# Kernel tuning notes

Measured on AMD Instinct MI355X. Metric: run time of the kernel, lower is better.

## Reference

```python
import jax, jax.numpy as jnp
import numpy as np

B, S, H = 128, 1000, 256


def setup_inputs() -> dict:
    key = jax.random.key(0)
    ks = jax.random.split(key, 15)
    sc = 1.0 / np.sqrt(H)
    f = lambda k, shape: (jax.random.normal(k, shape, jnp.float32) * sc)
    return dict(
        static_hidden=jax.random.normal(ks[0], (B, S, H), jnp.float32),
        state_embedding=jax.random.normal(ks[1], (B, 1, H), jnp.float32),
        decoder_hidden=jax.random.normal(ks[2], (B, 1, H), jnp.float32),
        target_hidden=jax.random.normal(ks[3], (B, 1, H), jnp.float32),
        last_hh=jax.random.normal(ks[4], (1, B, H), jnp.float32),
        W_ih=f(ks[5], (3 * H, H)),
        W_hh=f(ks[6], (3 * H, H)),
        b_ih=f(ks[7], (3 * H,)),
        b_hh=f(ks[8], (3 * H,)),
        v_attn_enc=f(ks[9], (H,)),
        W_attn_enc=f(ks[10], (H, 2 * H)),
        v_attn_tgt=f(ks[11], (H,)),
        W_attn_tgt=f(ks[12], (H, 2 * H)),
        v_ptr=f(ks[13], (H,)),
        W_ptr=f(ks[14], (H, 3 * H)),
    )


def _attention(static, dec, v, W):
    # static: [B,S,H], dec: [B,1,H] -> softmax attention over S
    hid = jnp.concatenate([static, jnp.broadcast_to(dec, static.shape)], axis=2)  # [B,S,2H]
    t = jnp.tanh(jnp.einsum('hk,bsk->bhs', W, hid))  # [B,H,S]
    return jax.nn.softmax(jnp.einsum('h,bhs->bs', v, t), axis=1)  # [B,S]


def _gru_step(x, h, Wih, Whh, bih, bhh):
    # single-layer single-step torch GRU semantics; x,h: [B,H]
    gi = x @ Wih.T + bih
    gh = h @ Whh.T + bhh
    ir, iz, ig = jnp.split(gi, 3, axis=-1)
    hr, hz, hg = jnp.split(gh, 3, axis=-1)
    r = jax.nn.sigmoid(ir + hr)
    z = jax.nn.sigmoid(iz + hz)
    n = jnp.tanh(ig + r * hg)
    return (1.0 - z) * n + z * h


def _pointer_branch(static, state_emb, attn, v, W):
    context = jnp.einsum('bs,bsh->bh', attn, static)[:, None, :]  # [B,1,H]
    energy = jnp.concatenate(
        [static,
         jnp.broadcast_to(context, static.shape),
         jnp.broadcast_to(state_emb, static.shape)], axis=2)  # [B,S,3H]
    return jnp.einsum('h,bhs->bs', v, jnp.tanh(jnp.einsum('hk,bsk->bhs', W, energy)))


def reference(static_hidden, state_embedding, decoder_hidden, target_hidden, last_hh,
              W_ih, W_hh, b_ih, b_hh,
              v_attn_enc, W_attn_enc, v_attn_tgt, W_attn_tgt, v_ptr, W_ptr):
    # GRU step (dropout is identity in eval / p=0.0)
    h_new = _gru_step(decoder_hidden[:, 0, :], last_hh[0], W_ih, W_hh, b_ih, b_hh)
    rnn_out = h_new[:, None, :]  # [B,1,H]
    last_hh_new = h_new[None]    # [1,B,H]

    enc_attn = _attention(static_hidden, rnn_out, v_attn_enc, W_attn_enc)
    probs = _pointer_branch(static_hidden, state_embedding, enc_attn, v_ptr, W_ptr)

    tgt_attn = _attention(static_hidden, target_hidden, v_attn_tgt, W_attn_tgt)
    # NOTE: original code reuses self.v / self.W (not v_target/W_taret) for the
    # target branch energy -- replicated faithfully.
    probs_target = _pointer_branch(static_hidden, state_embedding, tgt_attn, v_ptr, W_ptr)

    return (5.0 * probs + probs_target, last_hh_new)
```

## Files before the change

kernel.cpp:

```cpp
#include <hip/hip_runtime.h>
#include <hip/hip_bf16.h>
#include <stdint.h>
#include <stddef.h>

#define Bn 128
#define Sn 1000
#define SP 1024
#define Hn 256

typedef __bf16 bf16;
typedef __bf16 bf16x8 __attribute__((ext_vector_type(8)));
typedef __bf16 bf16x4 __attribute__((ext_vector_type(4)));
typedef __bf16 bf16x2 __attribute__((ext_vector_type(2)));
typedef float  f32x4  __attribute__((ext_vector_type(4)));

typedef __attribute__((address_space(1))) const unsigned int* gas1;
typedef __attribute__((address_space(3))) unsigned int* las3;

__device__ __forceinline__ float fast_tanh(float x){
  return 1.0f - 2.0f / (__expf(2.0f * x) + 1.0f);
}
__device__ __forceinline__ float fast_sigmoid(float x){
  return 1.0f / (1.0f + __expf(-x));
}
__device__ __forceinline__ float dot4(float4 a, float4 b){
  return a.x*b.x + a.y*b.y + a.z*b.z + a.w*b.w;
}

__global__ void k0a_convert(const float* __restrict__ stat, bf16* __restrict__ Abf){
  int p = blockIdx.x * 256 + threadIdx.x;
  int row = p >> 5;
  int ch  = p & 31;
  int s = row & (SP - 1);
  int b = row >> 10;
  float4 f0 = make_float4(0.f,0.f,0.f,0.f), f1 = f0;
  if (s < Sn){
    const float4* src = (const float4*)(stat + ((size_t)(b*Sn + s))*Hn + ch*8);
    f0 = src[0]; f1 = src[1];
  }
  bf16x8 v;
  v[0]=(bf16)f0.x; v[1]=(bf16)f0.y; v[2]=(bf16)f0.z; v[3]=(bf16)f0.w;
  v[4]=(bf16)f1.x; v[5]=(bf16)f1.y; v[6]=(bf16)f1.z; v[7]=(bf16)f1.w;
  *(bf16x8*)(Abf + (size_t)row*Hn + ch*8) = v;
}

__global__ void k0b_weights(const float* __restrict__ We, const float* __restrict__ Wt,
                            const float* __restrict__ Wp, bf16* __restrict__ Wcb){
  int t = blockIdx.x * 256 + threadIdx.x;
  int r = t >> 8, c = t & 255;
  float val;
  if (r < 256)       val = We[r*512 + c];
  else if (r < 512)  val = Wt[(r-256)*512 + c];
  else               val = Wp[(r-512)*768 + c];
  Wcb[t] = (bf16)val;
}

__global__ void k1_gru(const float* __restrict__ dec, const float* __restrict__ lhh,
                       const float* __restrict__ tgt, const float* __restrict__ se,
                       const float* __restrict__ Wih, const float* __restrict__ Whh,
                       const float* __restrict__ bih, const float* __restrict__ bhh,
                       const float* __restrict__ We,  const float* __restrict__ Wt,
                       const float* __restrict__ Wp,
                       float* __restrict__ out_hh, float* __restrict__ d_enc,
                       float* __restrict__ d_tgt,  float* __restrict__ c3){
  __shared__ __align__(16) float xs[256], hs[256], hn[256], ts[256], ss[256];
  int b = blockIdx.x, t = threadIdx.x;
  xs[t] = dec[b*256 + t];
  hs[t] = lhh[b*256 + t];
  ts[t] = tgt[b*256 + t];
  ss[t] = se[b*256 + t];
  __syncthreads();

  const float4* wir = (const float4*)(Wih + (size_t)t*256);
  const float4* wiz = (const float4*)(Wih + (size_t)(256+t)*256);
  const float4* wig = (const float4*)(Wih + (size_t)(512+t)*256);
  const float4* whr = (const float4*)(Whh + (size_t)t*256);
  const float4* whz = (const float4*)(Whh + (size_t)(256+t)*256);
  const float4* whg = (const float4*)(Whh + (size_t)(512+t)*256);
  float gir=0.f, giz=0.f, gig=0.f, ghr=0.f, ghz=0.f, ghg=0.f;
  #pragma unroll 4
  for (int k=0;k<64;k++){
    float4 xv = ((const float4*)xs)[k];
    float4 hv = ((const float4*)hs)[k];
    gir += dot4(wir[k], xv);
    giz += dot4(wiz[k], xv);
    gig += dot4(wig[k], xv);
    ghr += dot4(whr[k], hv);
    ghz += dot4(whz[k], hv);
    ghg += dot4(whg[k], hv);
  }
  gir += bih[t];      ghr += bhh[t];
  giz += bih[256+t];  ghz += bhh[256+t];
  gig += bih[512+t];  ghg += bhh[512+t];
  float r = fast_sigmoid(gir + ghr);
  float z = fast_sigmoid(giz + ghz);
  float n = fast_tanh(gig + r*ghg);
  float h = (1.f - z)*n + z*hs[t];
  hn[t] = h;
  out_hh[b*256 + t] = h;
  __syncthreads();

  const float4* we2 = (const float4*)(We + (size_t)t*512 + 256);
  const float4* wt2 = (const float4*)(Wt + (size_t)t*512 + 256);
  const float4* wp3 = (const float4*)(Wp + (size_t)t*768 + 512);
  float de=0.f, dt=0.f, cv=0.f;
  #pragma unroll 4
  for (int k=0;k<64;k++){
    float4 hv = ((const float4*)hn)[k];
    float4 tv = ((const float4*)ts)[k];
    float4 sv = ((const float4*)ss)[k];
    de += dot4(we2[k], hv);
    dt += dot4(wt2[k], tv);
    cv += dot4(wp3[k], sv);
  }
  d_enc[b*256 + t] = de;
  d_tgt[b*256 + t] = dt;
  c3[b*256 + t]    = cv;
}

__global__ __launch_bounds__(256) void k2_gemm(
    const bf16* __restrict__ Abf, const bf16* __restrict__ Wcb,
    const float* __restrict__ d_enc, const float* __restrict__ d_tgt,
    const float* __restrict__ c3, const float* __restrict__ v_enc,
    const float* __restrict__ v_tgt,
    float* __restrict__ sc_e, float* __restrict__ sc_t,
    bf16* __restrict__ Aptr){
  __shared__ __align__(16) bf16 As[64*256];
  __shared__ __align__(16) bf16 Bs[128*64];
  __shared__ float scoreE[64], scoreT[64];
  int tid = threadIdx.x;
  int w = tid >> 6, l = tid & 63;
  int st = blockIdx.x, b = blockIdx.y;
  int wm = (w & 1) * 32, wn = (w >> 1) * 64;
  int lm = l & 15, q = l >> 4;

  if (tid < 64) scoreE[tid] = 0.f;
  else if (tid < 128) scoreT[tid-64] = 0.f;

  {
    const bf16* gA = Abf + ((size_t)(b*SP + st*64)) * Hn;
    int rl = w*2 + (l >> 5);
    int ch = l & 31;
    #pragma unroll
    for (int is = 0; is < 8; is++){
      int row = is*8 + rl;
      int sc_ = ch ^ (row & 7);
      __builtin_amdgcn_global_load_lds((gas1)(gA + (size_t)row*256 + sc_*8),
                                       (las3)(&As[(is*8 + w*2)*256]), 16, 0, 0);
    }
  }

  int rB8 = w*8 + (l >> 3);
  int chB = l & 7;

  for (int nc = 0; nc < 6; nc++){
    f32x4 acc[2][4];
    #pragma unroll
    for (int i=0;i<2;i++)
      #pragma unroll
      for (int j=0;j<4;j++) acc[i][j] = (f32x4){0.f,0.f,0.f,0.f};

    for (int kt = 0; kt < 4; kt++){
      __syncthreads();
      #pragma unroll
      for (int is = 0; is < 4; is++){
        int row = is*32 + rB8;
        int sc_ = chB ^ (row & 7);
        __builtin_amdgcn_global_load_lds((gas1)(Wcb + ((size_t)(nc*128 + row))*256 + kt*64 + sc_*8),
                                         (las3)(&Bs[(is*32 + w*8)*64]), 16, 0, 0);
      }
      __syncthreads();
      #pragma unroll
      for (int kk = 0; kk < 64; kk += 32){
        bf16x8 af[2], bfr[4];
        int cA = kt*8 + (kk >> 3) + q;
        int cB = (kk >> 3) + q;
        #pragma unroll
        for (int i=0;i<2;i++){
          int rA = wm + i*16 + lm;
          af[i] = *(const bf16x8*)(&As[rA*256 + ((cA ^ (rA & 7)) << 3)]);
        }
        #pragma unroll
        for (int j=0;j<4;j++){
          int rB = wn + j*16 + lm;
          bfr[j] = *(const bf16x8*)(&Bs[rB*64 + ((cB ^ (rB & 7)) << 3)]);
        }
        #pragma unroll
        for (int i=0;i<2;i++)
          #pragma unroll
          for (int j=0;j<4;j++)
            acc[i][j] = __builtin_amdgcn_mfma_f32_16x16x32_bf16(af[i], bfr[j], acc[i][j], 0, 0, 0);
      }
    }

    int hb = (nc & 1) * 128;
    if (nc < 4){
      const float* vv = (nc < 2) ? v_enc : v_tgt;
      const float* db = ((nc < 2) ? d_enc : d_tgt) + b*256;
      float* sc = (nc < 2) ? scoreE : scoreT;
      float vj[4], dj[4];
      #pragma unroll
      for (int j=0;j<4;j++){
        int hh = hb + wn + j*16 + lm;
        vj[j] = vv[hh]; dj[j] = db[hh];
      }
      #pragma unroll
      for (int i=0;i<2;i++){
        #pragma unroll
        for (int r=0;r<4;r++){
          float p = 0.f;
          #pragma unroll
          for (int j=0;j<4;j++) p += vj[j] * fast_tanh(acc[i][j][r] + dj[j]);
          p += __shfl_xor(p, 1);
          p += __shfl_xor(p, 2);
          p += __shfl_xor(p, 4);
          p += __shfl_xor(p, 8);
          if (lm == 0) atomicAdd(&sc[wm + i*16 + q*4 + r], p);
        }
      }
    } else {
      int hbp = (nc - 4) * 128;
      const float* c3b = c3 + b*256;
      float cv[4]; int hhj[4];
      #pragma unroll
      for (int j=0;j<4;j++){
        hhj[j] = hbp + wn + j*16 + lm;
        cv[j] = c3b[hhj[j]];
      }
      #pragma unroll
      for (int i=0;i<2;i++){
        #pragma unroll
        for (int r=0;r<4;r++){
          int row = wm + i*16 + q*4 + r;
          int gs = st*64 + row;
          if (gs < Sn){
            size_t rb = ((size_t)(b*Sn + gs))*256;
            #pragma unroll
            for (int j=0;j<4;j++)
              Aptr[rb + hhj[j]] = (bf16)(acc[i][j][r] + cv[j]);
          }
        }
      }
    }
  }

  __syncthreads();
  if (tid < 64)       sc_e[b*SP + st*64 + tid]      = scoreE[tid];
  else if (tid < 128) sc_t[b*SP + st*64 + tid - 64] = scoreT[tid-64];
}

__global__ __launch_bounds__(1024) void k3_ctx(
    const float* __restrict__ sc_e, const float* __restrict__ sc_t,
    const bf16* __restrict__ Abf,
    float* __restrict__ ctxPE, float* __restrict__ ctxPT){
  __shared__ float attE[1024], attT[1024];
  __shared__ float redE[16], redT[16];
  __shared__ float pe[8*256], pt[8*256];
  int b = blockIdx.x, sp = blockIdx.y, t = threadIdx.x;
  int wid = t >> 6, ln = t & 63;

  float vE = (t < Sn) ? sc_e[b*SP + t] : -1e30f;
  float vT = (t < Sn) ? sc_t[b*SP + t] : -1e30f;
  float mE = vE, mT = vT;
  #pragma unroll
  for (int o=1;o<64;o<<=1){ mE = fmaxf(mE, __shfl_xor(mE,o)); mT = fmaxf(mT, __shfl_xor(mT,o)); }
  if (ln == 0){ redE[wid] = mE; redT[wid] = mT; }
  __syncthreads();
  float ME = -1e30f, MT = -1e30f;
  #pragma unroll
  for (int i=0;i<16;i++){ ME = fmaxf(ME, redE[i]); MT = fmaxf(MT, redT[i]); }
  __syncthreads();
  float eE = (t < Sn) ? __expf(vE - ME) : 0.f;
  float eT = (t < Sn) ? __expf(vT - MT) : 0.f;
  float sE = eE, sT = eT;
  #pragma unroll
  for (int o=1;o<64;o<<=1){ sE += __shfl_xor(sE,o); sT += __shfl_xor(sT,o); }
  if (ln == 0){ redE[wid] = sE; redT[wid] = sT; }
  __syncthreads();
  float SE = 0.f, ST = 0.f;
  #pragma unroll
  for (int i=0;i<16;i++){ SE += redE[i]; ST += redT[i]; }
  attE[t] = eE / SE;
  attT[t] = eT / ST;
  __syncthreads();

  int sh = t >> 7, hp = t & 127;
  const bf16* base = Abf + ((size_t)(b*SP + sp*500))*Hn + hp*2;
  float aE0=0.f, aE1=0.f, aT0=0.f, aT1=0.f;
  #pragma unroll 4
  for (int i=0;i<63;i++){
    int sl = sh + 8*i;
    if (sl < 500){
      int s = sp*500 + sl;
      float wE = attE[s], wT = attT[s];
      bf16x2 pr = *(const bf16x2*)(base + (size_t)sl*Hn);
      float p0 = (float)pr[0], p1 = (float)pr[1];
      aE0 += wE*p0; aE1 += wE*p1;
      aT0 += wT*p0; aT1 += wT*p1;
    }
  }
  pe[sh*256 + hp*2] = aE0; pe[sh*256 + hp*2+1] = aE1;
  pt[sh*256 + hp*2] = aT0; pt[sh*256 + hp*2+1] = aT1;
  __syncthreads();
  if (t < 256){
    float s = 0.f;
    #pragma unroll
    for (int i=0;i<8;i++) s += pe[i*256 + t];
    ctxPE[((size_t)(sp*Bn + b))*256 + t] = s;
  } else if (t < 512){
    int tt = t - 256;
    float s = 0.f;
    #pragma unroll
    for (int i=0;i<8;i++) s += pt[i*256 + tt];
    ctxPT[((size_t)(sp*Bn + b))*256 + tt] = s;
  }
}

__global__ void k3c_c2(const float* __restrict__ ctxPE, const float* __restrict__ ctxPT,
                       const float* __restrict__ Wp,
                       float* __restrict__ c2e, float* __restrict__ c2t){
  __shared__ __align__(16) float ctx[256];
  int b = blockIdx.x, which = blockIdx.y, t = threadIdx.x;
  const float* cp = which ? ctxPT : ctxPE;
  ctx[t] = cp[(size_t)b*256 + t] + cp[((size_t)(Bn + b))*256 + t];
  __syncthreads();
  const float4* wrow = (const float4*)(Wp + (size_t)t*768 + 256);
  float acc = 0.f;
  #pragma unroll 4
  for (int k=0;k<64;k++) acc += dot4(wrow[k], ((const float4*)ctx)[k]);
  (which ? c2t : c2e)[b*256 + t] = acc;
}

__global__ void k4_final(const bf16* __restrict__ Aptr, const float* __restrict__ c2e,
                         const float* __restrict__ c2t, const float* __restrict__ vp,
                         float* __restrict__ out){
  int w = threadIdx.x >> 6, l = threadIdx.x & 63;
  int row = blockIdx.x*4 + w;
  int b = row / 1000;
  const bf16* ap = Aptr + (size_t)row*Hn + l*4;
  bf16x4 av = *(const bf16x4*)ap;
  float4 ce = *(const float4*)(c2e + b*256 + l*4);
  float4 ct = *(const float4*)(c2t + b*256 + l*4);
  float4 vv = *(const float4*)(vp + l*4);
  float a0 = (float)av[0], a1 = (float)av[1], a2 = (float)av[2], a3 = (float)av[3];
  float pe = vv.x*fast_tanh(a0+ce.x) + vv.y*fast_tanh(a1+ce.y)
           + vv.z*fast_tanh(a2+ce.z) + vv.w*fast_tanh(a3+ce.w);
  float pt = vv.x*fast_tanh(a0+ct.x) + vv.y*fast_tanh(a1+ct.y)
           + vv.z*fast_tanh(a2+ct.z) + vv.w*fast_tanh(a3+ct.w);
  #pragma unroll
  for (int o=1;o<64;o<<=1){
    pe += __shfl_xor(pe, o);
    pt += __shfl_xor(pt, o);
  }
  if (l == 0) out[row] = 5.0f*pe + pt;
}

extern "C" void kernel_launch(void* const* d_in, const int* in_sizes, int n_in,
                              void* d_out, int out_size, void* d_ws, size_t ws_size,
                              hipStream_t stream){
  const float* stat = (const float*)d_in[0];
  const float* se   = (const float*)d_in[1];
  const float* dec  = (const float*)d_in[2];
  const float* tgt  = (const float*)d_in[3];
  const float* lhh  = (const float*)d_in[4];
  const float* Wih  = (const float*)d_in[5];
  const float* Whh  = (const float*)d_in[6];
  const float* bih  = (const float*)d_in[7];
  const float* bhh  = (const float*)d_in[8];
  const float* vEnc = (const float*)d_in[9];
  const float* WEnc = (const float*)d_in[10];
  const float* vTgt = (const float*)d_in[11];
  const float* WTgt = (const float*)d_in[12];
  const float* vPtr = (const float*)d_in[13];
  const float* WPtr = (const float*)d_in[14];
  float* out = (float*)d_out;

  char* wsp = (char*)d_ws;
  bf16*  Abf  = (bf16*)(wsp);
  bf16*  Aptr = (bf16*)(wsp + 67108864);
  bf16*  Wcb  = (bf16*)(wsp + 132644864);
  float* scE  = (float*)(wsp + 133038080);
  float* scT  = (float*)(wsp + 133562368);
  float* dEnc = (float*)(wsp + 134086656);
  float* dTgt = (float*)(wsp + 134217728);
  float* c3   = (float*)(wsp + 134348800);
  float* c2e  = (float*)(wsp + 134479872);
  float* c2t  = (float*)(wsp + 134610944);
  float* ctxPE= (float*)(wsp + 134742016);
  float* ctxPT= (float*)(wsp + 135004160);

  hipLaunchKernelGGL(k0a_convert, dim3(16384), dim3(256), 0, stream, stat, Abf);
  hipLaunchKernelGGL(k0b_weights, dim3(768), dim3(256), 0, stream, WEnc, WTgt, WPtr, Wcb);
  hipLaunchKernelGGL(k1_gru, dim3(128), dim3(256), 0, stream,
                     dec, lhh, tgt, se, Wih, Whh, bih, bhh, WEnc, WTgt, WPtr,
                     out + Bn*Sn, dEnc, dTgt, c3);
  hipLaunchKernelGGL(k2_gemm, dim3(16, 128), dim3(256), 0, stream,
                     Abf, Wcb, dEnc, dTgt, c3, vEnc, vTgt, scE, scT, Aptr);
  hipLaunchKernelGGL(k3_ctx, dim3(128, 2), dim3(1024), 0, stream,
                     scE, scT, Abf, ctxPE, ctxPT);
  hipLaunchKernelGGL(k3c_c2, dim3(128, 2), dim3(256), 0, stream,
                     ctxPE, ctxPT, WPtr, c2e, c2t);
  hipLaunchKernelGGL(k4_final, dim3(32000), dim3(256), 0, stream,
                     Aptr, c2e, c2t, vPtr, out);
}
```

Measured before the change: 464.1 us.

## Recompute pointer projection in final GEMM instead of materializing Aptr

The pointer-branch projection of static_hidden is no longer written to a bf16 intermediate and re-read. A second MFMA kernel recomputes it from the bf16 static tile and fuses the tanh/v-reduction for both branches straight into the output. The context reduction and Wp context projection are merged into one kernel per batch. The GRU kernel now uses one wave per output row with shuffle reductions, and the GEMMs read B fragments directly from global memory instead of staging them in LDS. This trades a 64 MB intermediate write/read and two launches for a second pass over the static tile and redundant B loads.

```diff
diff --git a/kernel.cpp b/kernel.cpp
--- a/kernel.cpp
+++ b/kernel.cpp
@@ -25,6 +25,11 @@
 }
 __device__ __forceinline__ float dot4(float4 a, float4 b){
   return a.x*b.x + a.y*b.y + a.z*b.z + a.w*b.w;
+}
+__device__ __forceinline__ float wave_reduce(float v){
+  #pragma unroll
+  for (int o=1;o<64;o<<=1) v += __shfl_xor(v, o);
+  return v;
 }
 
 __global__ void k0a_convert(const float* __restrict__ stat, bf16* __restrict__ Abf){
@@ -55,87 +60,76 @@
   Wcb[t] = (bf16)val;
 }
 
-__global__ void k1_gru(const float* __restrict__ dec, const float* __restrict__ lhh,
-                       const float* __restrict__ tgt, const float* __restrict__ se,
-                       const float* __restrict__ Wih, const float* __restrict__ Whh,
-                       const float* __restrict__ bih, const float* __restrict__ bhh,
-                       const float* __restrict__ We,  const float* __restrict__ Wt,
-                       const float* __restrict__ Wp,
-                       float* __restrict__ out_hh, float* __restrict__ d_enc,
-                       float* __restrict__ d_tgt,  float* __restrict__ c3){
-  __shared__ __align__(16) float xs[256], hs[256], hn[256], ts[256], ss[256];
+__global__ __launch_bounds__(1024) void k1_gru(
+    const float* __restrict__ dec, const float* __restrict__ lhh,
+    const float* __restrict__ tgt, const float* __restrict__ se,
+    const float* __restrict__ Wih, const float* __restrict__ Whh,
+    const float* __restrict__ bih, const float* __restrict__ bhh,
+    const float* __restrict__ We,  const float* __restrict__ Wt,
+    const float* __restrict__ Wp,
+    float* __restrict__ out_hh, float* __restrict__ d_enc,
+    float* __restrict__ d_tgt,  float* __restrict__ c3){
+  __shared__ __align__(16) float xs[256], hs[256], ts[256], ss[256], hn[256];
+  __shared__ float gi[768], gh[768];
   int b = blockIdx.x, t = threadIdx.x;
-  xs[t] = dec[b*256 + t];
-  hs[t] = lhh[b*256 + t];
-  ts[t] = tgt[b*256 + t];
-  ss[t] = se[b*256 + t];
-  __syncthreads();
-
-  const float4* wir = (const float4*)(Wih + (size_t)t*256);
-  const float4* wiz = (const float4*)(Wih + (size_t)(256+t)*256);
-  const float4* wig = (const float4*)(Wih + (size_t)(512+t)*256);
-  const float4* whr = (const float4*)(Whh + (size_t)t*256);
-  const float4* whz = (const float4*)(Whh + (size_t)(256+t)*256);
-  const float4* whg = (const float4*)(Whh + (size_t)(512+t)*256);
-  float gir=0.f, giz=0.f, gig=0.f, ghr=0.f, ghz=0.f, ghg=0.f;
-  #pragma unroll 4
-  for (int k=0;k<64;k++){
-    float4 xv = ((const float4*)xs)[k];
-    float4 hv = ((const float4*)hs)[k];
-    gir += dot4(wir[k], xv);
-    giz += dot4(wiz[k], xv);
-    gig += dot4(wig[k], xv);
-    ghr += dot4(whr[k], hv);
-    ghz += dot4(whz[k], hv);
-    ghg += dot4(whg[k], hv);
-  }
-  gir += bih[t];      ghr += bhh[t];
-  giz += bih[256+t];  ghz += bhh[256+t];
-  gig += bih[512+t];  ghg += bhh[512+t];
-  float r = fast_sigmoid(gir + ghr);
-  float z = fast_sigmoid(giz + ghz);
-  float n = fast_tanh(gig + r*ghg);
-  float h = (1.f - z)*n + z*hs[t];
-  hn[t] = h;
-  out_hh[b*256 + t] = h;
-  __syncthreads();
-
-  const float4* we2 = (const float4*)(We + (size_t)t*512 + 256);
-  const float4* wt2 = (const float4*)(Wt + (size_t)t*512 + 256);
-  const float4* wp3 = (const float4*)(Wp + (size_t)t*768 + 512);
-  float de=0.f, dt=0.f, cv=0.f;
-  #pragma unroll 4
-  for (int k=0;k<64;k++){
-    float4 hv = ((const float4*)hn)[k];
-    float4 tv = ((const float4*)ts)[k];
-    float4 sv = ((const float4*)ss)[k];
-    de += dot4(we2[k], hv);
-    dt += dot4(wt2[k], tv);
-    cv += dot4(wp3[k], sv);
-  }
-  d_enc[b*256 + t] = de;
-  d_tgt[b*256 + t] = dt;
-  c3[b*256 + t]    = cv;
-}
-
-__global__ __launch_bounds__(256) void k2_gemm(
+  int wid = t >> 6, ln = t & 63;
+  if (t < 256){
+    xs[t] = dec[b*256 + t]; hs[t] = lhh[b*256 + t];
+    ts[t] = tgt[b*256 + t]; ss[t] = se[b*256 + t];
+  }
+  __syncthreads();
+  #pragma unroll 2
+  for (int k = 0; k < 96; k++){
+    int vr = k*16 + wid;
+    const float* wr; const float* xv; 
+    int r;
+    if (vr < 768){ r = vr;      wr = Wih + (size_t)r*256; xv = xs; }
+    else         { r = vr-768;  wr = Whh + (size_t)r*256; xv = hs; }
+    float d = dot4(((const float4*)wr)[ln], ((const float4*)xv)[ln]);
+    d = wave_reduce(d);
+    if (ln == 0){
+      if (vr < 768) gi[r] = d + bih[r];
+      else          gh[r] = d + bhh[r];
+    }
+  }
+  __syncthreads();
+  if (t < 256){
+    float r = fast_sigmoid(gi[t] + gh[t]);
+    float z = fast_sigmoid(gi[256+t] + gh[256+t]);
+    float n = fast_tanh(gi[512+t] + r*gh[512+t]);
+    float h = (1.f - z)*n + z*hs[t];
+    hn[t] = h;
+    out_hh[b*256 + t] = h;
+  }
+  __syncthreads();
+  #pragma unroll 2
+  for (int k = 0; k < 48; k++){
+    int vr = k*16 + wid;
+    const float* wr; const float* xv; float* dst; int r;
+    if (vr < 256)      { r = vr;     wr = We + (size_t)r*512 + 256; xv = hn; dst = d_enc; }
+    else if (vr < 512) { r = vr-256; wr = Wt + (size_t)r*512 + 256; xv = ts; dst = d_tgt; }
+    else               { r = vr-512; wr = Wp + (size_t)r*768 + 512; xv = ss; dst = c3; }
+    float d = dot4(((const float4*)wr)[ln], ((const float4*)xv)[ln]);
+    d = wave_reduce(d);
+    if (ln == 0) dst[b*256 + r] = d;
+  }
+}
+
+__global__ __launch_bounds__(256) void k2a_scores(
     const bf16* __restrict__ Abf, const bf16* __restrict__ Wcb,
     const float* __restrict__ d_enc, const float* __restrict__ d_tgt,
-    const float* __restrict__ c3, const float* __restrict__ v_enc,
-    const float* __restrict__ v_tgt,
-    float* __restrict__ sc_e, float* __restrict__ sc_t,
-    bf16* __restrict__ Aptr){
+    const float* __restrict__ v_enc, const float* __restrict__ v_tgt,
+    float* __restrict__ sc_e, float* __restrict__ sc_t){
   __shared__ __align__(16) bf16 As[64*256];
-  __shared__ __align__(16) bf16 Bs[128*64];
-  __shared__ float scoreE[64], scoreT[64];
+  __shared__ float pS[2][64];
   int tid = threadIdx.x;
   int w = tid >> 6, l = tid & 63;
   int st = blockIdx.x, b = blockIdx.y;
   int wm = (w & 1) * 32, wn = (w >> 1) * 64;
   int lm = l & 15, q = l >> 4;
 
-  if (tid < 64) scoreE[tid] = 0.f;
-  else if (tid < 128) scoreT[tid-64] = 0.f;
+  if (tid < 64) pS[0][tid] = 0.f;
+  else if (tid < 128) pS[1][tid-64] = 0.f;
 
   {
     const bf16* gA = Abf + ((size_t)(b*SP + st*64)) * Hn;
@@ -149,114 +143,73 @@
                                        (las3)(&As[(is*8 + w*2)*256]), 16, 0, 0);
     }
   }
-
-  int rB8 = w*8 + (l >> 3);
-  int chB = l & 7;
-
-  for (int nc = 0; nc < 6; nc++){
+  __syncthreads();
+
+  #pragma unroll
+  for (int nc = 0; nc < 4; nc++){
     f32x4 acc[2][4];
     #pragma unroll
     for (int i=0;i<2;i++)
       #pragma unroll
       for (int j=0;j<4;j++) acc[i][j] = (f32x4){0.f,0.f,0.f,0.f};
-
-    for (int kt = 0; kt < 4; kt++){
-      __syncthreads();
-      #pragma unroll
-      for (int is = 0; is < 4; is++){
-        int row = is*32 + rB8;
-        int sc_ = chB ^ (row & 7);
-        __builtin_amdgcn_global_load_lds((gas1)(Wcb + ((size_t)(nc*128 + row))*256 + kt*64 + sc_*8),
-                                         (las3)(&Bs[(is*32 + w*8)*64]), 16, 0, 0);
+    const bf16* Bb = Wcb + ((size_t)(nc*128 + wn + lm))*256 + q*8;
+    #pragma unroll
+    for (int ks = 0; ks < 8; ks++){
+      bf16x8 bfr[4], af[2];
+      #pragma unroll
+      for (int j=0;j<4;j++) bfr[j] = *(const bf16x8*)(Bb + (size_t)(j*16)*256 + ks*32);
+      #pragma unroll
+      for (int i=0;i<2;i++){
+        int rA = wm + i*16 + lm;
+        int c = (ks*4 + q) ^ (rA & 7);
+        af[i] = *(const bf16x8*)(&As[rA*256 + c*8]);
       }
-      __syncthreads();
-      #pragma unroll
-      for (int kk = 0; kk < 64; kk += 32){
-        bf16x8 af[2], bfr[4];
-        int cA = kt*8 + (kk >> 3) + q;
-        int cB = (kk >> 3) + q;
+      #pragma unroll
+      for (int i=0;i<2;i++)
         #pragma unroll
-        for (int i=0;i<2;i++){
-          int rA = wm + i*16 + lm;
-          af[i] = *(const bf16x8*)(&As[rA*256 + ((cA ^ (rA & 7)) << 3)]);
-        }
+        for (int j=0;j<4;j++)
+          acc[i][j] = __builtin_amdgcn_mfma_f32_16x16x32_bf16(af[i], bfr[j], acc[i][j], 0, 0, 0);
+    }
+    int var = nc >> 1;
+    int hb = (nc & 1) * 128;
+    const float* vv = var ? v_tgt : v_enc;
+    const float* db = (var ? d_tgt : d_enc) + b*256;
+    float vj[4], dj[4];
+    #pragma unroll
+    for (int j=0;j<4;j++){
+      int hh = hb + wn + j*16 + lm;
+      vj[j] = vv[hh]; dj[j] = db[hh];
+    }
+    #pragma unroll
+    for (int i=0;i<2;i++){
+      #pragma unroll
+      for (int r=0;r<4;r++){
+        float p = 0.f;
         #pragma unroll
-        for (int j=0;j<4;j++){
-          int rB = wn + j*16 + lm;
-          bfr[j] = *(const bf16x8*)(&Bs[rB*64 + ((cB ^ (rB & 7)) << 3)]);
-        }
-        #pragma unroll
-        for (int i=0;i<2;i++)
-          #pragma unroll
-          for (int j=0;j<4;j++)
-            acc[i][j] = __builtin_amdgcn_mfma_f32_16x16x32_bf16(af[i], bfr[j], acc[i][j], 0, 0, 0);
+        for (int j=0;j<4;j++) p += vj[j] * fast_tanh(acc[i][j][r] + dj[j]);
+        p += __shfl_xor(p, 1);
+        p += __shfl_xor(p, 2);
+        p += __shfl_xor(p, 4);
+        p += __shfl_xor(p, 8);
+        if (lm == 0) atomicAdd(&pS[var][wm + i*16 + q*4 + r], p);
       }
     }
-
-    int hb = (nc & 1) * 128;
-    if (nc < 4){
-      const float* vv = (nc < 2) ? v_enc : v_tgt;
-      const float* db = ((nc < 2) ? d_enc : d_tgt) + b*256;
-      float* sc = (nc < 2) ? scoreE : scoreT;
-      float vj[4], dj[4];
-      #pragma unroll
-      for (int j=0;j<4;j++){
-        int hh = hb + wn + j*16 + lm;
-        vj[j] = vv[hh]; dj[j] = db[hh];
-      }
-      #pragma unroll
-      for (int i=0;i<2;i++){
-        #pragma unroll
-        for (int r=0;r<4;r++){
-          float p = 0.f;
-          #pragma unroll
-          for (int j=0;j<4;j++) p += vj[j] * fast_tanh(acc[i][j][r] + dj[j]);
-          p += __shfl_xor(p, 1);
-          p += __shfl_xor(p, 2);
-          p += __shfl_xor(p, 4);
-          p += __shfl_xor(p, 8);
-          if (lm == 0) atomicAdd(&sc[wm + i*16 + q*4 + r], p);
-        }
-      }
-    } else {
-      int hbp = (nc - 4) * 128;
-      const float* c3b = c3 + b*256;
-      float cv[4]; int hhj[4];
-      #pragma unroll
-      for (int j=0;j<4;j++){
-        hhj[j] = hbp + wn + j*16 + lm;
-        cv[j] = c3b[hhj[j]];
-      }
-      #pragma unroll
-      for (int i=0;i<2;i++){
-        #pragma unroll
-        for (int r=0;r<4;r++){
-          int row = wm + i*16 + q*4 + r;
-          int gs = st*64 + row;
-          if (gs < Sn){
-            size_t rb = ((size_t)(b*Sn + gs))*256;
-            #pragma unroll
-            for (int j=0;j<4;j++)
-              Aptr[rb + hhj[j]] = (bf16)(acc[i][j][r] + cv[j]);
-          }
-        }
-      }
-    }
-  }
-
-  __syncthreads();
-  if (tid < 64)       sc_e[b*SP + st*64 + tid]      = scoreE[tid];
-  else if (tid < 128) sc_t[b*SP + st*64 + tid - 64] = scoreT[tid-64];
+  }
+  __syncthreads();
+  if (tid < 64)       sc_e[b*SP + st*64 + tid]      = pS[0][tid];
+  else if (tid < 128) sc_t[b*SP + st*64 + tid - 64] = pS[1][tid-64];
 }
 
 __global__ __launch_bounds__(1024) void k3_ctx(
     const float* __restrict__ sc_e, const float* __restrict__ sc_t,
-    const bf16* __restrict__ Abf,
-    float* __restrict__ ctxPE, float* __restrict__ ctxPT){
+    const bf16* __restrict__ Abf, const float* __restrict__ Wp,
+    const float* __restrict__ c3,
+    float* __restrict__ cE, float* __restrict__ cT){
   __shared__ float attE[1024], attT[1024];
   __shared__ float redE[16], redT[16];
-  __shared__ float pe[8*256], pt[8*256];
-  int b = blockIdx.x, sp = blockIdx.y, t = threadIdx.x;
+  __shared__ float pe[4][256], pt[4][256];
+  __shared__ __align__(16) float ctxE[256], ctxT[256];
+  int b = blockIdx.x, t = threadIdx.x;
   int wid = t >> 6, ln = t & 63;
 
   float vE = (t < Sn) ? sc_e[b*SP + t] : -1e30f;
@@ -284,75 +237,131 @@
   attT[t] = eT / ST;
   __syncthreads();
 
-  int sh = t >> 7, hp = t & 127;
-  const bf16* base = Abf + ((size_t)(b*SP + sp*500))*Hn + hp*2;
-  float aE0=0.f, aE1=0.f, aT0=0.f, aT1=0.f;
+  int sh = t >> 8, hp = t & 255;
+  const bf16* base = Abf + ((size_t)(b*SP + sh*250))*Hn + hp;
+  float aE = 0.f, aT = 0.f;
   #pragma unroll 4
-  for (int i=0;i<63;i++){
-    int sl = sh + 8*i;
-    if (sl < 500){
-      int s = sp*500 + sl;
-      float wE = attE[s], wT = attT[s];
-      bf16x2 pr = *(const bf16x2*)(base + (size_t)sl*Hn);
-      float p0 = (float)pr[0], p1 = (float)pr[1];
-      aE0 += wE*p0; aE1 += wE*p1;
-      aT0 += wT*p0; aT1 += wT*p1;
-    }
-  }
-  pe[sh*256 + hp*2] = aE0; pe[sh*256 + hp*2+1] = aE1;
-  pt[sh*256 + hp*2] = aT0; pt[sh*256 + hp*2+1] = aT1;
-  __syncthreads();
-  if (t < 256){
-    float s = 0.f;
-    #pragma unroll
-    for (int i=0;i<8;i++) s += pe[i*256 + t];
-    ctxPE[((size_t)(sp*Bn + b))*256 + t] = s;
-  } else if (t < 512){
-    int tt = t - 256;
-    float s = 0.f;
-    #pragma unroll
-    for (int i=0;i<8;i++) s += pt[i*256 + tt];
-    ctxPT[((size_t)(sp*Bn + b))*256 + tt] = s;
-  }
-}
-
-__global__ void k3c_c2(const float* __restrict__ ctxPE, const float* __restrict__ ctxPT,
-                       const float* __restrict__ Wp,
-                       float* __restrict__ c2e, float* __restrict__ c2t){
-  __shared__ __align__(16) float ctx[256];
-  int b = blockIdx.x, which = blockIdx.y, t = threadIdx.x;
-  const float* cp = which ? ctxPT : ctxPE;
-  ctx[t] = cp[(size_t)b*256 + t] + cp[((size_t)(Bn + b))*256 + t];
-  __syncthreads();
-  const float4* wrow = (const float4*)(Wp + (size_t)t*768 + 256);
-  float acc = 0.f;
-  #pragma unroll 4
-  for (int k=0;k<64;k++) acc += dot4(wrow[k], ((const float4*)ctx)[k]);
-  (which ? c2t : c2e)[b*256 + t] = acc;
-}
-
-__global__ void k4_final(const bf16* __restrict__ Aptr, const float* __restrict__ c2e,
-                         const float* __restrict__ c2t, const float* __restrict__ vp,
-                         float* __restrict__ out){
-  int w = threadIdx.x >> 6, l = threadIdx.x & 63;
-  int row = blockIdx.x*4 + w;
-  int b = row / 1000;
-  const bf16* ap = Aptr + (size_t)row*Hn + l*4;
-  bf16x4 av = *(const bf16x4*)ap;
-  float4 ce = *(const float4*)(c2e + b*256 + l*4);
-  float4 ct = *(const float4*)(c2t + b*256 + l*4);
-  float4 vv = *(const float4*)(vp + l*4);
-  float a0 = (float)av[0], a1 = (float)av[1], a2 = (float)av[2], a3 = (float)av[3];
-  float pe = vv.x*fast_tanh(a0+ce.x) + vv.y*fast_tanh(a1+ce.y)
-           + vv.z*fast_tanh(a2+ce.z) + vv.w*fast_tanh(a3+ce.w);
-  float pt = vv.x*fast_tanh(a0+ct.x) + vv.y*fast_tanh(a1+ct.y)
-           + vv.z*fast_tanh(a2+ct.z) + vv.w*fast_tanh(a3+ct.w);
-  #pragma unroll
-  for (int o=1;o<64;o<<=1){
-    pe += __shfl_xor(pe, o);
-    pt += __shfl_xor(pt, o);
-  }
-  if (l == 0) out[row] = 5.0f*pe + pt;
+  for (int i=0;i<250;i++){
+    float a = (float)base[(size_t)i*Hn];
+    int s = sh*250 + i;
+    aE += attE[s]*a; aT += attT[s]*a;
+  }
+  pe[sh][hp] = aE; pt[sh][hp] = aT;
+  __syncthreads();
+  if (t < 256)       ctxE[t]     = pe[0][t]+pe[1][t]+pe[2][t]+pe[3][t];
+  else if (t < 512){ int h=t-256; ctxT[h]  = pt[0][h]+pt[1][h]+pt[2][h]+pt[3][h]; }
+  __syncthreads();
+  if (t < 512){
+    int h = t & 255, var = t >> 8;
+    const float4* wrow = (const float4*)(Wp + (size_t)h*768 + 256);
+    const float4* cv = (const float4*)(var ? ctxT : ctxE);
+    float acc = 0.f;
+    #pragma unroll 4
+    for (int k=0;k<64;k++) acc += dot4(wrow[k], cv[k]);
+    (var ? cT : cE)[b*256 + h] = acc + c3[b*256 + h];
+  }
+}
+
+__global__ __launch_bounds__(256) void k2b_final(
+    const bf16* __restrict__ Abf, const bf16* __restrict__ Wcb,
+    const float* __restrict__ cE, const float* __restrict__ cT,
+    const float* __restrict__ v_ptr, float* __restrict__ out){
+  __shared__ __align__(16) bf16 As[64*256];
+  __shared__ float pE[64], pT[64];
+  int tid = threadIdx.x;
+  int w = tid >> 6, l = tid & 63;
+  int st = blockIdx.x, b = blockIdx.y;
+  int wm = (w & 1) * 32, wn = (w >> 1) * 64;
+  int lm = l & 15, q = l >> 4;
+
+  if (tid < 64) pE[tid] = 0.f;
+  else if (tid < 128) pT[tid-64] = 0.f;
+
+  {
+    const bf16* gA = Abf + ((size_t)(b*SP + st*64)) * Hn;
+    int rl = w*2 + (l >> 5);
+    int ch = l & 31;
+    #pragma unroll
+    for (int is = 0; is < 8; is++){
+      int row = is*8 + rl;
+      int sc_ = ch ^ (row & 7);
+      __builtin_amdgcn_global_load_lds((gas1)(gA + (size_t)row*256 + sc_*8),
+                                       (las3)(&As[(is*8 + w*2)*256]), 16, 0, 0);
+    }
+  }
+  __syncthreads();
+
+  float peA[2][4], ptA[2][4];
+  #pragma unroll
+  for (int i=0;i<2;i++)
+    #pragma unroll
+    for (int r=0;r<4;r++){ peA[i][r]=0.f; ptA[i][r]=0.f; }
+
+  #pragma unroll
+  for (int nc = 0; nc < 2; nc++){
+    f32x4 acc[2][4];
+    #pragma unroll
+    for (int i=0;i<2;i++)
+      #pragma unroll
+      for (int j=0;j<4;j++) acc[i][j] = (f32x4){0.f,0.f,0.f,0.f};
+    const bf16* Bb = Wcb + ((size_t)((4+nc)*128 + wn + lm))*256 + q*8;
+    #pragma unroll
+    for (int ks = 0; ks < 8; ks++){
+      bf16x8 bfr[4], af[2];
+      #pragma unroll
+      for (int j=0;j<4;j++) bfr[j] = *(const bf16x8*)(Bb + (size_t)(j*16)*256 + ks*32);
+      #pragma unroll
+      for (int i=0;i<2;i++){
+        int rA = wm + i*16 + lm;
+        int c = (ks*4 + q) ^ (rA & 7);
+        af[i] = *(const bf16x8*)(&As[rA*256 + c*8]);
+      }
+      #pragma unroll
+      for (int i=0;i<2;i++)
+        #pragma unroll
+        for (int j=0;j<4;j++)
+          acc[i][j] = __builtin_amdgcn_mfma_f32_16x16x32_bf16(af[i], bfr[j], acc[i][j], 0, 0, 0);
+    }
+    float vj[4], ej[4], tj[4];
+    #pragma unroll
+    for (int j=0;j<4;j++){
+      int hh = nc*128 + wn + j*16 + lm;
+      vj[j] = v_ptr[hh];
+      ej[j] = cE[b*256 + hh];
+      tj[j] = cT[b*256 + hh];
+    }
+    #pragma unroll
+    for (int i=0;i<2;i++)
+      #pragma unroll
+      for (int r=0;r<4;r++){
+        #pragma unroll
+        for (int j=0;j<4;j++){
+          peA[i][r] += vj[j] * fast_tanh(acc[i][j][r] + ej[j]);
+          ptA[i][r] += vj[j] * fast_tanh(acc[i][j][r] + tj[j]);
+        }
+      }
+  }
+  #pragma unroll
+  for (int i=0;i<2;i++){
+    #pragma unroll
+    for (int r=0;r<4;r++){
+      float pe = peA[i][r], pt = ptA[i][r];
+      pe += __shfl_xor(pe, 1); pt += __shfl_xor(pt, 1);
+      pe += __shfl_xor(pe, 2); pt += __shfl_xor(pt, 2);
+      pe += __shfl_xor(pe, 4); pt += __shfl_xor(pt, 4);
+      pe += __shfl_xor(pe, 8); pt += __shfl_xor(pt, 8);
+      if (lm == 0){
+        int row = wm + i*16 + q*4 + r;
+        atomicAdd(&pE[row], pe);
+        atomicAdd(&pT[row], pt);
+      }
+    }
+  }
+  __syncthreads();
+  if (tid < 64){
+    int s = st*64 + tid;
+    if (s < Sn) out[b*Sn + s] = 5.0f*pE[tid] + pT[tid];
+  }
 }
 
 extern "C" void kernel_launch(void* const* d_in, const int* in_sizes, int n_in,
@@ -377,29 +386,24 @@
 
   char* wsp = (char*)d_ws;
   bf16*  Abf  = (bf16*)(wsp);
-  bf16*  Aptr = (bf16*)(wsp + 67108864);
-  bf16*  Wcb  = (bf16*)(wsp + 132644864);
-  float* scE  = (float*)(wsp + 133038080);
-  float* scT  = (float*)(wsp + 133562368);
-  float* dEnc = (float*)(wsp + 134086656);
-  float* dTgt = (float*)(wsp + 134217728);
-  float* c3   = (float*)(wsp + 134348800);
-  float* c2e  = (float*)(wsp + 134479872);
-  float* c2t  = (float*)(wsp + 134610944);
-  float* ctxPE= (float*)(wsp + 134742016);
-  float* ctxPT= (float*)(wsp + 135004160);
+  bf16*  Wcb  = (bf16*)(wsp + 67108864);
+  float* scE  = (float*)(wsp + 67502080);
+  float* scT  = (float*)(wsp + 68026368);
+  float* dEnc = (float*)(wsp + 68550656);
+  float* dTgt = (float*)(wsp + 68681728);
+  float* c3   = (float*)(wsp + 68812800);
+  float* cE   = (float*)(wsp + 68943872);
+  float* cT   = (float*)(wsp + 69074944);
 
   hipLaunchKernelGGL(k0a_convert, dim3(16384), dim3(256), 0, stream, stat, Abf);
   hipLaunchKernelGGL(k0b_weights, dim3(768), dim3(256), 0, stream, WEnc, WTgt, WPtr, Wcb);
-  hipLaunchKernelGGL(k1_gru, dim3(128), dim3(256), 0, stream,
+  hipLaunchKernelGGL(k1_gru, dim3(128), dim3(1024), 0, stream,
                      dec, lhh, tgt, se, Wih, Whh, bih, bhh, WEnc, WTgt, WPtr,
                      out + Bn*Sn, dEnc, dTgt, c3);
-  hipLaunchKernelGGL(k2_gemm, dim3(16, 128), dim3(256), 0, stream,
-                     Abf, Wcb, dEnc, dTgt, c3, vEnc, vTgt, scE, scT, Aptr);
-  hipLaunchKernelGGL(k3_ctx, dim3(128, 2), dim3(1024), 0, stream,
-                     scE, scT, Abf, ctxPE, ctxPT);
-  hipLaunchKernelGGL(k3c_c2, dim3(128, 2), dim3(256), 0, stream,
-                     ctxPE, ctxPT, WPtr, c2e, c2t);
-  hipLaunchKernelGGL(k4_final, dim3(32000), dim3(256), 0, stream,
-                     Aptr, c2e, c2t, vPtr, out);
-}
+  hipLaunchKernelGGL(k2a_scores, dim3(16, 128), dim3(256), 0, stream,
+                     Abf, Wcb, dEnc, dTgt, vEnc, vTgt, scE, scT);
+  hipLaunchKernelGGL(k3_ctx, dim3(128), dim3(1024), 0, stream,
+                     scE, scT, Abf, WPtr, c3, cE, cT);
+  hipLaunchKernelGGL(k2b_final, dim3(16, 128), dim3(256), 0, stream,
+                     Abf, Wcb, cE, cT, vPtr, out);
+}
```

After: 589.2 us. 1.27x slower.
